# Kernel tuning notes

Hardware: AMD Instinct MI355X
Metric: run time of the kernel (lower is better)

Reference implementation:

```python
import jax, jax.numpy as jnp
import numpy as np

DEGREE = 5
A = 1.0
B = 1.0
IN_F = 1024
OUT_F = 1024
BATCH = 8192


def setup_inputs() -> dict:
    key = jax.random.key(0)
    k1, k2, k3, k4 = jax.random.split(key, 4)
    x = jax.random.normal(k1, (BATCH, IN_F), dtype=jnp.float32)
    # base_weight ~ kaiming-uniform-ish scale
    bound_w = 1.0 / np.sqrt(IN_F)
    base_weight = jax.random.uniform(k2, (OUT_F, IN_F), dtype=jnp.float32,
                                     minval=-bound_w, maxval=bound_w)
    std = 1.0 / (IN_F * np.sqrt(DEGREE + 1))
    jacobi_coeffs = std * jax.random.normal(k3, (OUT_F, IN_F, DEGREE + 1), dtype=jnp.float32)
    bias = jax.random.uniform(k4, (OUT_F,), dtype=jnp.float32, minval=-bound_w, maxval=bound_w)
    return {"x": x, "base_weight": base_weight, "jacobi_coeffs": jacobi_coeffs, "bias": bias}


def _jacobi_polynomials(x):
    # x: (batch, in_features) -> (batch, in_features, DEGREE+1)
    t = jnp.tanh(x)
    polys = [jnp.ones_like(t)]
    if DEGREE >= 1:
        polys.append(0.5 * (2.0 * (A + 1.0) * t + (A - B)))
    for k in range(2, DEGREE + 1):
        # recurrence coefficients (matching torch loop where k = written index)
        alpha_n = 2.0 * k * (k + A + B) * (2 * k + A + B - 2)
        beta_n = (2 * k + A + B - 1) * (A ** 2 - B ** 2)
        gamma_n = (2 * k + A + B - 2) * (2 * k + A + B - 1) * (2 * k + A + B)
        delta_n = 2.0 * (k + A - 1) * (k + B - 1) * (2 * k + A + B)
        Acoef = (beta_n + alpha_n * t) / gamma_n
        Bcoef = delta_n / gamma_n
        polys.append(Acoef * polys[k - 1] - Bcoef * polys[k - 2])
    return jnp.stack(polys, axis=-1)


def reference(x, base_weight, jacobi_coeffs, bias):
    # base branch: SiLU then linear
    base_out = jax.nn.silu(x) @ base_weight.T  # (b, out)
    # jacobi branch
    P = _jacobi_polynomials(x)  # (b, in, deg+1)
    jac_out = jnp.einsum('bik,oik->bo', P, jacobi_coeffs)
    return base_out + jac_out + bias
```

## Files before the change

### kernel.cpp

```cpp
#include <hip/hip_runtime.h>
#include <hip/hip_bf16.h>
#include <cstdint>
#include <cstddef>

#define BATCH   8192
#define IN_F    1024
#define OUT_F   1024
#define KAUG    (6 * 1024)
#define NSTEP   64

typedef __bf16 bf16x8 __attribute__((ext_vector_type(8)));
typedef float  f32x4  __attribute__((ext_vector_type(4)));

static constexpr size_t WAUG_B    = (size_t)OUT_F * KAUG * 2;
static constexpr size_t BIAS2_OFF = WAUG_B;

constexpr float M1_1 = 2.0f;
constexpr float M3_1 = -1.0714285714f;
constexpr float M5_1 =  0.5812890813f;
constexpr float M2_2 =  1.0666666667f;
constexpr float M4_2 = -1.0455026455f;
constexpr float M3_3 =  0.5714285714f;
constexpr float M5_3 = -0.8141735129f;
constexpr float M4_4 =  0.3047619048f;
constexpr float M5_5 =  0.1616161616f;
constexpr float M2_0 = -0.4f;
constexpr float M4_0 =  0.1777777778f;

__device__ __forceinline__ unsigned short f2bf(float f)
{
    __hip_bfloat16 h = __float2bfloat16(f);
    return *(unsigned short*)&h;
}
__device__ __forceinline__ unsigned pack2(float lo, float hi)
{
    return (unsigned)f2bf(lo) | ((unsigned)f2bf(hi) << 16);
}
__device__ __forceinline__ unsigned cvt_pk(float lo, float hi)
{
    unsigned r;
    asm("v_cvt_pk_bf16_f32 %0, %1, %2" : "=v"(r) : "v"(lo), "v"(hi));
    return r;
}

__global__ void prep_w(const float* __restrict__ W,
                       const float* __restrict__ C,
                       const float* __restrict__ bias,
                       __hip_bfloat16* __restrict__ Waug,
                       float* __restrict__ bias2)
{
    const int o = blockIdx.x;
    const int tid = threadIdx.x;

    __shared__ __align__(16) float cs[IN_F * 6];
    __shared__ float red[4];

    const float4* C4  = (const float4*)(C + (size_t)o * IN_F * 6);
    float4*       cs4 = (float4*)cs;
#pragma unroll
    for (int k = 0; k < 6; ++k) cs4[tid + k * 256] = C4[tid + k * 256];

    const float4 wv = ((const float4*)(W + (size_t)o * IN_F))[tid];
    const float w4[4] = {wv.x, wv.y, wv.z, wv.w};

    __syncthreads();

    float f[24];
#pragma unroll
    for (int q = 0; q < 6; ++q) {
        const float4 v = cs4[tid * 6 + q];
        f[q * 4 + 0] = v.x; f[q * 4 + 1] = v.y; f[q * 4 + 2] = v.z; f[q * 4 + 3] = v.w;
    }

    unsigned pk[12];
    float s = 0.f;
#pragma unroll
    for (int q = 0; q < 4; ++q) {
        const float c0 = f[q * 6 + 0], c1 = f[q * 6 + 1], c2 = f[q * 6 + 2];
        const float c3 = f[q * 6 + 3], c4 = f[q * 6 + 4], c5 = f[q * 6 + 5];
        const float cp1 = M1_1 * c1 + M3_1 * c3 + M5_1 * c5;
        const float cp2 = M2_2 * c2 + M4_2 * c4;
        const float cp3 = M3_3 * c3 + M5_3 * c5;
        const float cp4 = M4_4 * c4;
        const float cp5 = M5_5 * c5;
        s += c0 + M2_0 * c2 + M4_0 * c4;
        pk[q * 3 + 0] = pack2(w4[q], cp1);
        pk[q * 3 + 1] = pack2(cp2,   cp3);
        pk[q * 3 + 2] = pack2(cp4,   cp5);
    }

#pragma unroll
    for (int off = 32; off > 0; off >>= 1) s += __shfl_down(s, off, 64);
    if ((tid & 63) == 0) red[tid >> 6] = s;

    __syncthreads();
    uint4* csU = (uint4*)cs;
    csU[tid * 3 + 0] = make_uint4(pk[0], pk[1], pk[2],  pk[3]);
    csU[tid * 3 + 1] = make_uint4(pk[4], pk[5], pk[6],  pk[7]);
    csU[tid * 3 + 2] = make_uint4(pk[8], pk[9], pk[10], pk[11]);
    __syncthreads();

    uint4* out4 = (uint4*)(Waug + (size_t)o * KAUG);
#pragma unroll
    for (int k = 0; k < 3; ++k) out4[tid + k * 256] = csU[tid + k * 256];

    if (tid == 0) bias2[o] = bias[o] + red[0] + red[1] + red[2] + red[3];
}

__device__ __forceinline__ void async_load16(const void* g, void* l)
{
    __builtin_amdgcn_global_load_lds(
        (const __attribute__((address_space(1))) void*)g,
        (__attribute__((address_space(3))) void*)l,
        16, 0, 0);
}

#define ASB_B   53248
#define BSB_B   24576
#define AS_TOT  (2 * ASB_B)
#define SMEM_B  (AS_TOT + 2 * BSB_B)

__global__ __launch_bounds__(512, 2)
void gemm_kan(const float* __restrict__ X,
              const __hip_bfloat16* __restrict__ Waug,
              const float* __restrict__ bias2,
              float* __restrict__ out)
{
    extern __shared__ __align__(16) char smem[];

    const int tid  = threadIdx.x;
    const int lane = tid & 63;
    const int wave = tid >> 6;
    const int wm = wave >> 1, wn = wave & 1;
    const int mBase = blockIdx.x * 256;
    const int nBase = blockIdx.y * 128;

    const float* gx = X + (size_t)(mBase + (tid >> 1)) * IN_F + (tid & 1) * 8;
    char* const aw = smem + (tid >> 1) * 208 + (tid & 1) * 96;

    const __hip_bfloat16* gB[3]; int lB[3];
#pragma unroll
    for (int q = 0; q < 3; ++q) {
        const int ci = (q * 8 + wave) * 64 + lane;
        const int br = ci / 12, bc = ci - br * 12;
        gB[q] = Waug + (size_t)(nBase + br) * KAUG + bc * 8;
        lB[q] = AS_TOT + (q * 8 + wave) * 1024;
    }

    const int quad = lane >> 4, mr = lane & 15;
    const int aoff = (wm * 64 + mr) * 13 + quad;
    const int boff = (AS_TOT / 16) + (wn * 64 + mr) * 12 + quad;

    f32x4 acc[4][4] = {};

    {
#pragma unroll
        for (int q = 0; q < 3; ++q) async_load16(gB[q], smem + lB[q]);
        const float4 x0 = *(const float4*)(gx);
        const float4 x1 = *(const float4*)(gx + 4);
        const float xs[8] = {x0.x, x0.y, x0.z, x0.w, x1.x, x1.y, x1.z, x1.w};
        unsigned pk[24];
#pragma unroll
        for (int e = 0; e < 8; ++e) {
            const float x  = xs[e];
            const float v  = __expf(fminf(-x, 43.f));
            const float sg = __builtin_amdgcn_rcpf(1.f + v);
            const float s  = x * sg;
            const float u  = v * v;
            const float tt = (1.f - u) * __builtin_amdgcn_rcpf(1.f + u);
            const float t2 = tt * tt, t3 = t2 * tt, t4 = t2 * t2, t5 = t4 * tt;
            pk[e * 3 + 0] = cvt_pk(s,  tt);
            pk[e * 3 + 1] = cvt_pk(t2, t3);
            pk[e * 3 + 2] = cvt_pk(t4, t5);
        }
#pragma unroll
        for (int j = 0; j < 6; ++j)
            *(uint4*)(aw + j * 16) = make_uint4(pk[j * 4], pk[j * 4 + 1],
                                                pk[j * 4 + 2], pk[j * 4 + 3]);
    }
    __syncthreads();

#pragma unroll 1
    for (int t = 0; t < NSTEP; ++t) {
        if (t + 1 < NSTEP) {
            const int nsel = (t + 1) & 1;
#pragma unroll
            for (int q = 0; q < 3; ++q)
                async_load16(gB[q] + (size_t)(t + 1) * 96,
                             smem + lB[q] + nsel * BSB_B);
        }
        float4 xn0 = {}, xn1 = {};
        if (t + 1 < NSTEP) {
            xn0 = *(const float4*)(gx + (size_t)(t + 1) * 16);
            xn1 = *(const float4*)(gx + (size_t)(t + 1) * 16 + 4);
        }

        const bf16x8* V = (const bf16x8*)smem;
        const int ab = aoff + (t & 1) * (ASB_B / 16);
        const int bb = boff + (t & 1) * (BSB_B / 16);
#pragma unroll
        for (int kc = 0; kc < 3; ++kc) {
            bf16x8 a[4], b[4];
#pragma unroll
            for (int t4 = 0; t4 < 4; ++t4) a[t4] = V[ab + t4 * 208 + kc * 4];
#pragma unroll
            for (int t4 = 0; t4 < 4; ++t4) b[t4] = V[bb + t4 * 192 + kc * 4];
#pragma unroll
            for (int i = 0; i < 4; ++i)
#pragma unroll
                for (int jj = 0; jj < 4; ++jj)
                    acc[i][jj] = __builtin_amdgcn_mfma_f32_16x16x32_bf16(
                        a[i], b[jj], acc[i][jj], 0, 0, 0);
        }

        if (t + 1 < NSTEP) {
            const float xs[8] = {xn0.x, xn0.y, xn0.z, xn0.w, xn1.x, xn1.y, xn1.z, xn1.w};
            unsigned pk[24];
#pragma unroll
            for (int e = 0; e < 8; ++e) {
                const float x  = xs[e];
                const float v  = __expf(fminf(-x, 43.f));
                const float sg = __builtin_amdgcn_rcpf(1.f + v);
                const float s  = x * sg;
                const float u  = v * v;
                const float tt = (1.f - u) * __builtin_amdgcn_rcpf(1.f + u);
                const float t2 = tt * tt, t3 = t2 * tt, t4 = t2 * t2, t5 = t4 * tt;
                pk[e * 3 + 0] = cvt_pk(s,  tt);
                pk[e * 3 + 1] = cvt_pk(t2, t3);
                pk[e * 3 + 2] = cvt_pk(t4, t5);
            }
            char* const asd = aw + ((t + 1) & 1) * ASB_B;
#pragma unroll
            for (int j = 0; j < 6; ++j)
                *(uint4*)(asd + j * 16) = make_uint4(pk[j * 4], pk[j * 4 + 1],
                                                     pk[j * 4 + 2], pk[j * 4 + 3]);
        }
        __syncthreads();
    }

#pragma unroll
    for (int i = 0; i < 4; ++i) {
#pragma unroll
        for (int jj = 0; jj < 4; ++jj) {
            const int col = nBase + wn * 64 + jj * 16 + mr;
            const float b2 = bias2[col];
#pragma unroll
            for (int r = 0; r < 4; ++r) {
                const int row = mBase + wm * 64 + i * 16 + quad * 4 + r;
                out[(size_t)row * OUT_F + col] = acc[i][jj][r] + b2;
            }
        }
    }
}


extern "C" void kernel_launch(void* const* d_in, const int* in_sizes, int n_in,
                              void* d_out, int out_size, void* d_ws, size_t ws_size,
                              hipStream_t stream)
{
    (void)out_size; (void)ws_size;
    const float* x    = (const float*)d_in[0];
    const float* W    = (const float*)d_in[1];
    const float* C    = (const float*)d_in[2];
    const float* bias = (const float*)d_in[3];
    for (int i = 0; i < n_in; ++i) {
        if      (in_sizes[i] == BATCH * IN_F)     x    = (const float*)d_in[i];
        else if (in_sizes[i] == OUT_F * IN_F)     W    = (const float*)d_in[i];
        else if (in_sizes[i] == OUT_F * IN_F * 6) C    = (const float*)d_in[i];
        else if (in_sizes[i] == OUT_F)            bias = (const float*)d_in[i];
    }
    float* out = (float*)d_out;
    char* ws = (char*)d_ws;
    __hip_bfloat16* Waug  = (__hip_bfloat16*)ws;
    float*          bias2 = (float*)(ws + BIAS2_OFF);

    static bool smem_attr_done = false;
    if (!smem_attr_done) {
        (void)hipFuncSetAttribute((const void*)gemm_kan,
                                  hipFuncAttributeMaxDynamicSharedMemorySize,
                                  SMEM_B);
        smem_attr_done = true;
    }

    prep_w<<<dim3(OUT_F), dim3(256), 0, stream>>>(W, C, bias, Waug, bias2);
    gemm_kan<<<dim3(BATCH / 256, OUT_F / 128), dim3(512), SMEM_B, stream>>>(
        x, Waug, bias2, out);
}
```

Baseline: 210.0 us.

## Load weight fragments directly from global into registers instead of LDS staging

```diff
diff --git a/kernel.cpp b/kernel.cpp
--- a/kernel.cpp
+++ b/kernel.cpp
@@ -107,18 +107,8 @@
     if (tid == 0) bias2[o] = bias[o] + red[0] + red[1] + red[2] + red[3];
 }
 
-__device__ __forceinline__ void async_load16(const void* g, void* l)
-{
-    __builtin_amdgcn_global_load_lds(
-        (const __attribute__((address_space(1))) void*)g,
-        (__attribute__((address_space(3))) void*)l,
-        16, 0, 0);
-}
-
 #define ASB_B   53248
-#define BSB_B   24576
-#define AS_TOT  (2 * ASB_B)
-#define SMEM_B  (AS_TOT + 2 * BSB_B)
+#define SMEM_B  (2 * ASB_B)
 
 __global__ __launch_bounds__(512, 2)
 void gemm_kan(const float* __restrict__ X,
@@ -138,24 +128,17 @@
     const float* gx = X + (size_t)(mBase + (tid >> 1)) * IN_F + (tid & 1) * 8;
     char* const aw = smem + (tid >> 1) * 208 + (tid & 1) * 96;
 
-    const __hip_bfloat16* gB[3]; int lB[3];
-#pragma unroll
-    for (int q = 0; q < 3; ++q) {
-        const int ci = (q * 8 + wave) * 64 + lane;
-        const int br = ci / 12, bc = ci - br * 12;
-        gB[q] = Waug + (size_t)(nBase + br) * KAUG + bc * 8;
-        lB[q] = AS_TOT + (q * 8 + wave) * 1024;
-    }
-
     const int quad = lane >> 4, mr = lane & 15;
     const int aoff = (wm * 64 + mr) * 13 + quad;
-    const int boff = (AS_TOT / 16) + (wn * 64 + mr) * 12 + quad;
+
+    const __hip_bfloat16* pB[4];
+#pragma unroll
+    for (int t4 = 0; t4 < 4; ++t4)
+        pB[t4] = Waug + (size_t)(nBase + wn * 64 + t4 * 16 + mr) * KAUG + quad * 8;
 
     f32x4 acc[4][4] = {};
 
     {
-#pragma unroll
-        for (int q = 0; q < 3; ++q) async_load16(gB[q], smem + lB[q]);
         const float4 x0 = *(const float4*)(gx);
         const float4 x1 = *(const float4*)(gx + 4);
         const float xs[8] = {x0.x, x0.y, x0.z, x0.w, x1.x, x1.y, x1.z, x1.w};
@@ -168,10 +151,10 @@
             const float s  = x * sg;
             const float u  = v * v;
             const float tt = (1.f - u) * __builtin_amdgcn_rcpf(1.f + u);
-            const float t2 = tt * tt, t3 = t2 * tt, t4 = t2 * t2, t5 = t4 * tt;
+            const float t2 = tt * tt, t3 = t2 * tt, t4v = t2 * t2, t5 = t4v * tt;
             pk[e * 3 + 0] = cvt_pk(s,  tt);
             pk[e * 3 + 1] = cvt_pk(t2, t3);
-            pk[e * 3 + 2] = cvt_pk(t4, t5);
+            pk[e * 3 + 2] = cvt_pk(t4v, t5);
         }
 #pragma unroll
         for (int j = 0; j < 6; ++j)
@@ -182,13 +165,13 @@
 
 #pragma unroll 1
     for (int t = 0; t < NSTEP; ++t) {
-        if (t + 1 < NSTEP) {
-            const int nsel = (t + 1) & 1;
-#pragma unroll
-            for (int q = 0; q < 3; ++q)
-                async_load16(gB[q] + (size_t)(t + 1) * 96,
-                             smem + lB[q] + nsel * BSB_B);
-        }
+        bf16x8 fb[4][3];
+#pragma unroll
+        for (int t4 = 0; t4 < 4; ++t4)
+#pragma unroll
+            for (int kc = 0; kc < 3; ++kc)
+                fb[t4][kc] = *(const bf16x8*)(pB[t4] + kc * 32);
+
         float4 xn0 = {}, xn1 = {};
         if (t + 1 < NSTEP) {
             xn0 = *(const float4*)(gx + (size_t)(t + 1) * 16);
@@ -197,20 +180,17 @@
 
         const bf16x8* V = (const bf16x8*)smem;
         const int ab = aoff + (t & 1) * (ASB_B / 16);
-        const int bb = boff + (t & 1) * (BSB_B / 16);
 #pragma unroll
         for (int kc = 0; kc < 3; ++kc) {
-            bf16x8 a[4], b[4];
+            bf16x8 a[4];
 #pragma unroll
             for (int t4 = 0; t4 < 4; ++t4) a[t4] = V[ab + t4 * 208 + kc * 4];
-#pragma unroll
-            for (int t4 = 0; t4 < 4; ++t4) b[t4] = V[bb + t4 * 192 + kc * 4];
 #pragma unroll
             for (int i = 0; i < 4; ++i)
 #pragma unroll
                 for (int jj = 0; jj < 4; ++jj)
                     acc[i][jj] = __builtin_amdgcn_mfma_f32_16x16x32_bf16(
-                        a[i], b[jj], acc[i][jj], 0, 0, 0);
+                        a[i], fb[jj][kc], acc[i][jj], 0, 0, 0);
         }
 
         if (t + 1 < NSTEP) {
@@ -224,10 +204,10 @@
                 const float s  = x * sg;
                 const float u  = v * v;
                 const float tt = (1.f - u) * __builtin_amdgcn_rcpf(1.f + u);
-                const float t2 = tt * tt, t3 = t2 * tt, t4 = t2 * t2, t5 = t4 * tt;
+                const float t2 = tt * tt, t3 = t2 * tt, t4v = t2 * t2, t5 = t4v * tt;
                 pk[e * 3 + 0] = cvt_pk(s,  tt);
                 pk[e * 3 + 1] = cvt_pk(t2, t3);
-                pk[e * 3 + 2] = cvt_pk(t4, t5);
+                pk[e * 3 + 2] = cvt_pk(t4v, t5);
             }
             char* const asd = aw + ((t + 1) & 1) * ASB_B;
 #pragma unroll
@@ -235,6 +215,10 @@
                 *(uint4*)(asd + j * 16) = make_uint4(pk[j * 4], pk[j * 4 + 1],
                                                      pk[j * 4 + 2], pk[j * 4 + 3]);
         }
+
+#pragma unroll
+        for (int t4 = 0; t4 < 4; ++t4) pB[t4] += 96;
+
         __syncthreads();
     }
 
```

After: 344.9 us. 1.64x slower.
